# Kernel tuning notes

Hardware: AMD Instinct MI355X
Metric: run time of the kernel (lower is better)

The kernel has to match this reference:

```python
import jax, jax.numpy as jnp
import numpy as np

B, S, D, H = 4, 2048, 1024, 16
DH = D // H


def setup_inputs() -> dict:
    key = jax.random.key(0)
    ks = jax.random.split(key, 12)
    inv = 1.0 / np.sqrt(D)
    inp = {
        "queries": jax.random.normal(ks[0], (B, S, D), jnp.float32),
        "keys": jax.random.normal(ks[1], (B, S, D), jnp.float32),
        "values": jax.random.normal(ks[2], (B, S, D), jnp.float32),
        # causal mask: 1.0 where attention is disallowed (strictly upper triangle)
        "mask": jnp.triu(jnp.ones((S, S), jnp.float32), k=1)[None, None, :, :],
        "Wq": jax.random.normal(ks[3], (D, D), jnp.float32) * inv,
        "bq": jnp.zeros((D,), jnp.float32),
        "Wk": jax.random.normal(ks[4], (D, D), jnp.float32) * inv,
        "bk": jnp.zeros((D,), jnp.float32),
        "Wv": jax.random.normal(ks[5], (D, D), jnp.float32) * inv,
        "bv": jnp.zeros((D,), jnp.float32),
        "Wo": jax.random.normal(ks[6], (D, D), jnp.float32) * inv,
        "bo": jnp.zeros((D,), jnp.float32),
    }
    return inp


def _split_heads(x):
    # [B, S, D] -> [B, H, S, DH]
    b, s, _ = x.shape
    return x.reshape(b, s, H, DH).transpose(0, 2, 1, 3)


def reference(queries, keys, values, mask, Wq, bq, Wk, bk, Wv, bv, Wo, bo):
    q = _split_heads(queries @ Wq + bq)
    k = _split_heads(keys @ Wk + bk)
    v = _split_heads(values @ Wv + bv)
    scores = jnp.einsum("bhqd,bhkd->bhqk", q, k) / jnp.sqrt(jnp.float32(DH))
    scores = scores + mask * -1e9
    attn = jax.nn.softmax(scores, axis=-1)
    ctx = jnp.einsum("bhqk,bhkd->bhqd", attn, v)  # [B,H,S,DH]
    ctx = ctx.transpose(0, 2, 1, 3).reshape(queries.shape[0], -1, D)
    return ctx @ Wo + bo
```

## Files before the change

### kernel.cpp

```cpp
#include <hip/hip_runtime.h>
#include <hip/hip_bf16.h>

#define S_LEN 2048
#define DMODEL 1024
#define NHEAD 16
#define DHEAD 64
#define BATCH 4
#define MTOT (BATCH * S_LEN)

typedef __attribute__((ext_vector_type(8))) short short8;
typedef __attribute__((ext_vector_type(8))) unsigned short ushort8;
typedef __attribute__((ext_vector_type(4))) float f32x4;

__device__ __forceinline__ unsigned short f2bf(float x) {
    unsigned int u = __float_as_uint(x);
    u += 0x7FFFu + ((u >> 16) & 1u);
    return (unsigned short)(u >> 16);
}

__global__ __launch_bounds__(256) void k_conv_bf16(const float* __restrict__ src,
                                                   unsigned short* __restrict__ dst, int n8) {
    int i = blockIdx.x * 256 + threadIdx.x;
    if (i >= n8) return;
    const float4* s4 = (const float4*)src;
    float4 a = s4[(size_t)i * 2];
    float4 b = s4[(size_t)i * 2 + 1];
    ushort8 v;
    v[0] = f2bf(a.x); v[1] = f2bf(a.y); v[2] = f2bf(a.z); v[3] = f2bf(a.w);
    v[4] = f2bf(b.x); v[5] = f2bf(b.y); v[6] = f2bf(b.z); v[7] = f2bf(b.w);
    *(ushort8*)(dst + (size_t)i * 8) = v;
}

__global__ __launch_bounds__(256) void k_transpose_w(const float* __restrict__ W0, const float* __restrict__ W1,
                                                     const float* __restrict__ W2, const float* __restrict__ W3,
                                                     unsigned short* __restrict__ T0, unsigned short* __restrict__ T1,
                                                     unsigned short* __restrict__ T2, unsigned short* __restrict__ T3) {
    const float* src; unsigned short* dst;
    switch (blockIdx.z) {
        case 0: src = W0; dst = T0; break;
        case 1: src = W1; dst = T1; break;
        case 2: src = W2; dst = T2; break;
        default: src = W3; dst = T3; break;
    }
    __shared__ float t[32][33];
    int tx = threadIdx.x & 31, ty = threadIdx.x >> 5;
    int n0 = blockIdx.x * 32, k0 = blockIdx.y * 32;
#pragma unroll
    for (int i = 0; i < 32; i += 8)
        t[ty + i][tx] = src[(size_t)(k0 + ty + i) * DMODEL + n0 + tx];
    __syncthreads();
#pragma unroll
    for (int i = 0; i < 32; i += 8)
        dst[(size_t)(n0 + ty + i) * DMODEL + k0 + tx] = f2bf(t[tx][ty + i]);
}

template <int OUT_FP32>
__global__ __launch_bounds__(256) void k_gemm_nt(const unsigned short* __restrict__ A,
                                                 const unsigned short* __restrict__ Bt,
                                                 const float* __restrict__ bias,
                                                 void* __restrict__ Cout,
                                                 int M, int N, int K, float alpha) {
    __shared__ unsigned short Al[128 * 32];
    __shared__ unsigned short Bl[128 * 32];
    int tid = threadIdx.x;
    int wid = tid >> 6;
    int lane = tid & 63;
    int lr = lane & 15, lg = lane >> 4;
    int bm = blockIdx.y * 128, bn = blockIdx.x * 128;
    int wm = (wid >> 1) * 64, wn = (wid & 1) * 64;

    f32x4 acc[4][4];
#pragma unroll
    for (int mt = 0; mt < 4; ++mt)
#pragma unroll
        for (int nt = 0; nt < 4; ++nt) acc[mt][nt] = (f32x4)0.0f;

    for (int k0 = 0; k0 < K; k0 += 32) {
#pragma unroll
        for (int i = 0; i < 2; ++i) {
            int c = (wid * 2 + i) * 64 + lane;
            int row = c >> 2, cc = c & 3;
            const unsigned short* ga = A + (size_t)(bm + row) * K + k0 + cc * 8;
            const unsigned short* gb = Bt + (size_t)(bn + row) * K + k0 + cc * 8;
            __builtin_amdgcn_global_load_lds((const __attribute__((address_space(1))) unsigned int*)ga,
                                             (__attribute__((address_space(3))) unsigned int*)(Al + (wid * 2 + i) * 512),
                                             16, 0, 0);
            __builtin_amdgcn_global_load_lds((const __attribute__((address_space(1))) unsigned int*)gb,
                                             (__attribute__((address_space(3))) unsigned int*)(Bl + (wid * 2 + i) * 512),
                                             16, 0, 0);
        }
        __syncthreads();

        short8 af[4], bf[4];
#pragma unroll
        for (int mt = 0; mt < 4; ++mt)
            af[mt] = *(const short8*)(Al + (wm + mt * 16 + lr) * 32 + lg * 8);
#pragma unroll
        for (int nt = 0; nt < 4; ++nt)
            bf[nt] = *(const short8*)(Bl + (wn + nt * 16 + lr) * 32 + lg * 8);
#pragma unroll
        for (int mt = 0; mt < 4; ++mt)
#pragma unroll
            for (int nt = 0; nt < 4; ++nt)
                acc[mt][nt] = __builtin_amdgcn_mfma_f32_16x16x32_bf16(af[mt], bf[nt], acc[mt][nt], 0, 0, 0);
        __syncthreads();
    }

#pragma unroll
    for (int nt = 0; nt < 4; ++nt) {
        int col = bn + wn + nt * 16 + lr;
        float bv = bias[col];
#pragma unroll
        for (int mt = 0; mt < 4; ++mt) {
#pragma unroll
            for (int r = 0; r < 4; ++r) {
                int row = bm + wm + mt * 16 + lg * 4 + r;
                float v = (acc[mt][nt][r] + bv) * alpha;
                if (OUT_FP32)
                    ((float*)Cout)[(size_t)row * N + col] = v;
                else
                    ((unsigned short*)Cout)[(size_t)row * N + col] = f2bf(v);
            }
        }
    }
}

__global__ __launch_bounds__(64, 2) void k_attn(const unsigned short* __restrict__ Qp,
                                                const unsigned short* __restrict__ Kp,
                                                const unsigned short* __restrict__ Vp,
                                                unsigned short* __restrict__ Ctx) {
    int lane = threadIdx.x & 63;
    int lr = lane & 15, lg = lane >> 4;
    int qb = blockIdx.x;
    int bh = blockIdx.y;
    int b = bh >> 4, h = bh & 15;
    size_t baserow = (size_t)b * S_LEN;
    int hcol = h * DHEAD;

    short8 qf[4][2];
#pragma unroll
    for (int qt = 0; qt < 4; ++qt)
#pragma unroll
        for (int ks = 0; ks < 2; ++ks)
            qf[qt][ks] = *(const short8*)(Qp + (baserow + qb * 64 + qt * 16 + lr) * DMODEL + hcol + ks * 32 + lg * 8);

    f32x4 ctx[4][4];
#pragma unroll
    for (int dt = 0; dt < 4; ++dt)
#pragma unroll
        for (int qt = 0; qt < 4; ++qt) ctx[dt][qt] = (f32x4)0.0f;

    float mrun[4], lrun[4];
#pragma unroll
    for (int qt = 0; qt < 4; ++qt) { mrun[qt] = -1e30f; lrun[qt] = 0.0f; }

    for (int kb = 0; kb <= qb; ++kb) {
        f32x4 s[4][4];
#pragma unroll
        for (int kt = 0; kt < 4; ++kt)
#pragma unroll
            for (int qt = 0; qt < 4; ++qt) s[kt][qt] = (f32x4)0.0f;

#pragma unroll
        for (int kt = 0; kt < 4; ++kt) {
            short8 kf[2];
#pragma unroll
            for (int ks = 0; ks < 2; ++ks)
                kf[ks] = *(const short8*)(Kp + (baserow + kb * 64 + kt * 16 + lr) * DMODEL + hcol + ks * 32 + lg * 8);
#pragma unroll
            for (int qt = 0; qt < 4; ++qt)
#pragma unroll
                for (int ks = 0; ks < 2; ++ks)
                    s[kt][qt] = __builtin_amdgcn_mfma_f32_16x16x32_bf16(kf[ks], qf[qt][ks], s[kt][qt], 0, 0, 0);
        }

        if (kb == qb) {
#pragma unroll
            for (int kt = 0; kt < 4; ++kt)
#pragma unroll
                for (int qt = 0; qt < 4; ++qt)
#pragma unroll
                    for (int r = 0; r < 4; ++r)
                        if (kt * 16 + lg * 4 + r > qt * 16 + lr) s[kt][qt][r] = -1e30f;
        }

        short8 pf[4][2];
#pragma unroll
        for (int qt = 0; qt < 4; ++qt) {
            float mx = -1e30f;
#pragma unroll
            for (int kt = 0; kt < 4; ++kt)
#pragma unroll
                for (int r = 0; r < 4; ++r) mx = fmaxf(mx, s[kt][qt][r]);
            mx = fmaxf(mx, __shfl_xor(mx, 16));
            mx = fmaxf(mx, __shfl_xor(mx, 32));
            float mnew = fmaxf(mrun[qt], mx);
            float scale = __expf(mrun[qt] - mnew);
            mrun[qt] = mnew;
            float rs = 0.0f;
#pragma unroll
            for (int kt = 0; kt < 4; ++kt)
#pragma unroll
                for (int r = 0; r < 4; ++r) {
                    float p = __expf(s[kt][qt][r] - mnew);
                    s[kt][qt][r] = p;
                    rs += p;
                }
            rs += __shfl_xor(rs, 16);
            rs += __shfl_xor(rs, 32);
            lrun[qt] = lrun[qt] * scale + rs;
#pragma unroll
            for (int dt = 0; dt < 4; ++dt)
#pragma unroll
                for (int r = 0; r < 4; ++r) ctx[dt][qt][r] *= scale;
#pragma unroll
            for (int ks = 0; ks < 2; ++ks)
#pragma unroll
                for (int j = 0; j < 8; ++j)
                    pf[qt][ks][j] = (short)f2bf(s[2 * ks + (j >> 2)][qt][j & 3]);
        }

        const unsigned short* vbase = Vp + (baserow + kb * 64) * DMODEL + hcol + lr;
#pragma unroll
        for (int dt = 0; dt < 4; ++dt) {
#pragma unroll
            for (int ks = 0; ks < 2; ++ks) {
                short8 vf;
#pragma unroll
                for (int j = 0; j < 8; ++j) {
                    int kk = 32 * ks + 16 * (j >> 2) + 4 * lg + (j & 3);
                    vf[j] = (short)vbase[(size_t)kk * DMODEL + dt * 16];
                }
#pragma unroll
                for (int qt = 0; qt < 4; ++qt)
                    ctx[dt][qt] = __builtin_amdgcn_mfma_f32_16x16x32_bf16(vf, pf[qt][ks], ctx[dt][qt], 0, 0, 0);
            }
        }
    }

#pragma unroll
    for (int qt = 0; qt < 4; ++qt) {
        float inv = 1.0f / lrun[qt];
#pragma unroll
        for (int dt = 0; dt < 4; ++dt) {
            unsigned int lo = (unsigned int)f2bf(ctx[dt][qt][0] * inv) | ((unsigned int)f2bf(ctx[dt][qt][1] * inv) << 16);
            unsigned int hi = (unsigned int)f2bf(ctx[dt][qt][2] * inv) | ((unsigned int)f2bf(ctx[dt][qt][3] * inv) << 16);
            uint2 vv; vv.x = lo; vv.y = hi;
            *(uint2*)(Ctx + (baserow + qb * 64 + qt * 16 + lr) * DMODEL + hcol + dt * 16 + lg * 4) = vv;
        }
    }
}

extern "C" void kernel_launch(void* const* d_in, const int* in_sizes, int n_in,
                              void* d_out, int out_size, void* d_ws, size_t ws_size,
                              hipStream_t stream) {
    const float* q_in = (const float*)d_in[0];
    const float* k_in = (const float*)d_in[1];
    const float* v_in = (const float*)d_in[2];
    const float* Wq = (const float*)d_in[4];
    const float* bq = (const float*)d_in[5];
    const float* Wk = (const float*)d_in[6];
    const float* bk = (const float*)d_in[7];
    const float* Wv = (const float*)d_in[8];
    const float* bv = (const float*)d_in[9];
    const float* Wo = (const float*)d_in[10];
    const float* bo = (const float*)d_in[11];

    char* ws = (char*)d_ws;
    const size_t SZ_ACT = (size_t)MTOT * DMODEL * 2;
    const size_t SZ_W = (size_t)DMODEL * DMODEL * 2;
    unsigned short* Xq = (unsigned short*)(ws);
    unsigned short* Xk = (unsigned short*)(ws + SZ_ACT);
    unsigned short* Xv = (unsigned short*)(ws + 2 * SZ_ACT);
    unsigned short* Tq = (unsigned short*)(ws + 3 * SZ_ACT);
    unsigned short* Tk = (unsigned short*)(ws + 3 * SZ_ACT + SZ_W);
    unsigned short* Tv = (unsigned short*)(ws + 3 * SZ_ACT + 2 * SZ_W);
    unsigned short* To = (unsigned short*)(ws + 3 * SZ_ACT + 3 * SZ_W);
    unsigned short* Qp = (unsigned short*)(ws + 3 * SZ_ACT + 4 * SZ_W);
    unsigned short* Kp = (unsigned short*)(ws + 4 * SZ_ACT + 4 * SZ_W);
    unsigned short* Vp = (unsigned short*)(ws + 5 * SZ_ACT + 4 * SZ_W);
    unsigned short* Cx = (unsigned short*)(ws + 6 * SZ_ACT + 4 * SZ_W);

    int n8 = MTOT * DMODEL / 8;
    k_conv_bf16<<<(n8 + 255) / 256, 256, 0, stream>>>(q_in, Xq, n8);
    k_conv_bf16<<<(n8 + 255) / 256, 256, 0, stream>>>(k_in, Xk, n8);
    k_conv_bf16<<<(n8 + 255) / 256, 256, 0, stream>>>(v_in, Xv, n8);
    k_transpose_w<<<dim3(32, 32, 4), 256, 0, stream>>>(Wq, Wk, Wv, Wo, Tq, Tk, Tv, To);

    dim3 gg(DMODEL / 128, MTOT / 128);
    k_gemm_nt<0><<<gg, 256, 0, stream>>>(Xq, Tq, bq, Qp, MTOT, DMODEL, DMODEL, 0.125f);
    k_gemm_nt<0><<<gg, 256, 0, stream>>>(Xk, Tk, bk, Kp, MTOT, DMODEL, DMODEL, 1.0f);
    k_gemm_nt<0><<<gg, 256, 0, stream>>>(Xv, Tv, bv, Vp, MTOT, DMODEL, DMODEL, 1.0f);

    k_attn<<<dim3(S_LEN / 64, BATCH * NHEAD), 64, 0, stream>>>(Qp, Kp, Vp, Cx);

    k_gemm_nt<1><<<gg, 256, 0, stream>>>(Cx, To, bo, d_out, MTOT, DMODEL, DMODEL, 1.0f);
}
```

Measured before the change: 465.2 us.

## Batch QKV GEMMs, store V transposed, reorder attention blocks, add setprio

Merges the three conversion kernels into one launch and the three projection GEMMs into a single grid-z launch with a swizzled tile order. The V projection is written transposed per head, so the attention kernel loads V fragments with vector loads instead of strided scalar gathers, and those loads are hoisted before the softmax. Attention blocks are remapped so the longest causal query blocks start first and heads are spread across XCDs, occupancy is raised to 3, and s_setprio wraps the MFMA bursts. The V epilogue now does scattered 2-byte stores along the sequence stride, which may slow that GEMM's output writes.

```diff
diff --git a/kernel.cpp b/kernel.cpp
--- a/kernel.cpp
+++ b/kernel.cpp
@@ -10,6 +10,7 @@
 
 typedef __attribute__((ext_vector_type(8))) short short8;
 typedef __attribute__((ext_vector_type(8))) unsigned short ushort8;
+typedef __attribute__((ext_vector_type(4))) unsigned short ushort4v;
 typedef __attribute__((ext_vector_type(4))) float f32x4;
 
 __device__ __forceinline__ unsigned short f2bf(float x) {
@@ -18,10 +19,14 @@
     return (unsigned short)(u >> 16);
 }
 
-__global__ __launch_bounds__(256) void k_conv_bf16(const float* __restrict__ src,
-                                                   unsigned short* __restrict__ dst, int n8) {
+__global__ __launch_bounds__(256) void k_conv3(const float* __restrict__ s0, const float* __restrict__ s1,
+                                               const float* __restrict__ s2,
+                                               unsigned short* __restrict__ d0, unsigned short* __restrict__ d1,
+                                               unsigned short* __restrict__ d2, int n8) {
     int i = blockIdx.x * 256 + threadIdx.x;
     if (i >= n8) return;
+    const float* src = blockIdx.y == 0 ? s0 : (blockIdx.y == 1 ? s1 : s2);
+    unsigned short* dst = blockIdx.y == 0 ? d0 : (blockIdx.y == 1 ? d1 : d2);
     const float4* s4 = (const float4*)src;
     float4 a = s4[(size_t)i * 2];
     float4 b = s4[(size_t)i * 2 + 1];
@@ -54,19 +59,30 @@
         dst[(size_t)(n0 + ty + i) * DMODEL + k0 + tx] = f2bf(t[tx][ty + i]);
 }
 
-template <int OUT_FP32>
-__global__ __launch_bounds__(256) void k_gemm_nt(const unsigned short* __restrict__ A,
-                                                 const unsigned short* __restrict__ Bt,
-                                                 const float* __restrict__ bias,
-                                                 void* __restrict__ Cout,
-                                                 int M, int N, int K, float alpha) {
+__global__ __launch_bounds__(256) void k_gemm_qkv(const unsigned short* __restrict__ Xq,
+                                                  const unsigned short* __restrict__ Xk,
+                                                  const unsigned short* __restrict__ Xv,
+                                                  const unsigned short* __restrict__ Tq,
+                                                  const unsigned short* __restrict__ Tk,
+                                                  const unsigned short* __restrict__ Tv,
+                                                  const float* __restrict__ bqp, const float* __restrict__ bkp,
+                                                  const float* __restrict__ bvp,
+                                                  unsigned short* __restrict__ Qp, unsigned short* __restrict__ Kp,
+                                                  unsigned short* __restrict__ Vt) {
+    int z = blockIdx.z;
+    const unsigned short* A = z == 0 ? Xq : (z == 1 ? Xk : Xv);
+    const unsigned short* Bt = z == 0 ? Tq : (z == 1 ? Tk : Tv);
+    const float* bias = z == 0 ? bqp : (z == 1 ? bkp : bvp);
+    float alpha = z == 0 ? 0.125f : 1.0f;
+
     __shared__ unsigned short Al[128 * 32];
     __shared__ unsigned short Bl[128 * 32];
     int tid = threadIdx.x;
-    int wid = tid >> 6;
-    int lane = tid & 63;
+    int wid = tid >> 6, lane = tid & 63;
     int lr = lane & 15, lg = lane >> 4;
-    int bm = blockIdx.y * 128, bn = blockIdx.x * 128;
+    int lin = blockIdx.y * 8 + blockIdx.x;
+    int tile = (lin & 7) * 64 + (lin >> 3);
+    int bm = (tile >> 3) * 128, bn = (tile & 7) * 128;
     int wm = (wid >> 1) * 64, wn = (wid & 1) * 64;
 
     f32x4 acc[4][4];
@@ -75,13 +91,13 @@
 #pragma unroll
         for (int nt = 0; nt < 4; ++nt) acc[mt][nt] = (f32x4)0.0f;
 
-    for (int k0 = 0; k0 < K; k0 += 32) {
+    for (int k0 = 0; k0 < DMODEL; k0 += 32) {
 #pragma unroll
         for (int i = 0; i < 2; ++i) {
             int c = (wid * 2 + i) * 64 + lane;
             int row = c >> 2, cc = c & 3;
-            const unsigned short* ga = A + (size_t)(bm + row) * K + k0 + cc * 8;
-            const unsigned short* gb = Bt + (size_t)(bn + row) * K + k0 + cc * 8;
+            const unsigned short* ga = A + (size_t)(bm + row) * DMODEL + k0 + cc * 8;
+            const unsigned short* gb = Bt + (size_t)(bn + row) * DMODEL + k0 + cc * 8;
             __builtin_amdgcn_global_load_lds((const __attribute__((address_space(1))) unsigned int*)ga,
                                              (__attribute__((address_space(3))) unsigned int*)(Al + (wid * 2 + i) * 512),
                                              16, 0, 0);
@@ -90,7 +106,6 @@
                                              16, 0, 0);
         }
         __syncthreads();
-
         short8 af[4], bf[4];
 #pragma unroll
         for (int mt = 0; mt < 4; ++mt)
@@ -98,11 +113,13 @@
 #pragma unroll
         for (int nt = 0; nt < 4; ++nt)
             bf[nt] = *(const short8*)(Bl + (wn + nt * 16 + lr) * 32 + lg * 8);
+        __builtin_amdgcn_s_setprio(1);
 #pragma unroll
         for (int mt = 0; mt < 4; ++mt)
 #pragma unroll
             for (int nt = 0; nt < 4; ++nt)
                 acc[mt][nt] = __builtin_amdgcn_mfma_f32_16x16x32_bf16(af[mt], bf[nt], acc[mt][nt], 0, 0, 0);
+        __builtin_amdgcn_s_setprio(0);
         __syncthreads();
     }
 
@@ -116,23 +133,96 @@
             for (int r = 0; r < 4; ++r) {
                 int row = bm + wm + mt * 16 + lg * 4 + r;
                 float v = (acc[mt][nt][r] + bv) * alpha;
-                if (OUT_FP32)
-                    ((float*)Cout)[(size_t)row * N + col] = v;
-                else
-                    ((unsigned short*)Cout)[(size_t)row * N + col] = f2bf(v);
+                if (z < 2) {
+                    unsigned short* dst = z == 0 ? Qp : Kp;
+                    dst[(size_t)row * DMODEL + col] = f2bf(v);
+                } else {
+                    int h = col >> 6, d = col & 63;
+                    int b = row >> 11, s = row & 2047;
+                    Vt[((size_t)(b * NHEAD + h) * DHEAD + d) * S_LEN + s] = f2bf(v);
+                }
             }
         }
     }
 }
 
-__global__ __launch_bounds__(64, 2) void k_attn(const unsigned short* __restrict__ Qp,
+__global__ __launch_bounds__(256) void k_gemm_out(const unsigned short* __restrict__ A,
+                                                  const unsigned short* __restrict__ Bt,
+                                                  const float* __restrict__ bias,
+                                                  float* __restrict__ Cout) {
+    __shared__ unsigned short Al[128 * 32];
+    __shared__ unsigned short Bl[128 * 32];
+    int tid = threadIdx.x;
+    int wid = tid >> 6, lane = tid & 63;
+    int lr = lane & 15, lg = lane >> 4;
+    int lin = blockIdx.y * 8 + blockIdx.x;
+    int tile = (lin & 7) * 64 + (lin >> 3);
+    int bm = (tile >> 3) * 128, bn = (tile & 7) * 128;
+    int wm = (wid >> 1) * 64, wn = (wid & 1) * 64;
+
+    f32x4 acc[4][4];
+#pragma unroll
+    for (int mt = 0; mt < 4; ++mt)
+#pragma unroll
+        for (int nt = 0; nt < 4; ++nt) acc[mt][nt] = (f32x4)0.0f;
+
+    for (int k0 = 0; k0 < DMODEL; k0 += 32) {
+#pragma unroll
+        for (int i = 0; i < 2; ++i) {
+            int c = (wid * 2 + i) * 64 + lane;
+            int row = c >> 2, cc = c & 3;
+            const unsigned short* ga = A + (size_t)(bm + row) * DMODEL + k0 + cc * 8;
+            const unsigned short* gb = Bt + (size_t)(bn + row) * DMODEL + k0 + cc * 8;
+            __builtin_amdgcn_global_load_lds((const __attribute__((address_space(1))) unsigned int*)ga,
+                                             (__attribute__((address_space(3))) unsigned int*)(Al + (wid * 2 + i) * 512),
+                                             16, 0, 0);
+            __builtin_amdgcn_global_load_lds((const __attribute__((address_space(1))) unsigned int*)gb,
+                                             (__attribute__((address_space(3))) unsigned int*)(Bl + (wid * 2 + i) * 512),
+                                             16, 0, 0);
+        }
+        __syncthreads();
+        short8 af[4], bf[4];
+#pragma unroll
+        for (int mt = 0; mt < 4; ++mt)
+            af[mt] = *(const short8*)(Al + (wm + mt * 16 + lr) * 32 + lg * 8);
+#pragma unroll
+        for (int nt = 0; nt < 4; ++nt)
+            bf[nt] = *(const short8*)(Bl + (wn + nt * 16 + lr) * 32 + lg * 8);
+        __builtin_amdgcn_s_setprio(1);
+#pragma unroll
+        for (int mt = 0; mt < 4; ++mt)
+#pragma unroll
+            for (int nt = 0; nt < 4; ++nt)
+                acc[mt][nt] = __builtin_amdgcn_mfma_f32_16x16x32_bf16(af[mt], bf[nt], acc[mt][nt], 0, 0, 0);
+        __builtin_amdgcn_s_setprio(0);
+        __syncthreads();
+    }
+
+#pragma unroll
+    for (int nt = 0; nt < 4; ++nt) {
+        int col = bn + wn + nt * 16 + lr;
+        float bv = bias[col];
+#pragma unroll
+        for (int mt = 0; mt < 4; ++mt)
+#pragma unroll
+            for (int r = 0; r < 4; ++r) {
+                int row = bm + wm + mt * 16 + lg * 4 + r;
+                Cout[(size_t)row * DMODEL + col] = acc[mt][nt][r] + bv;
+            }
+    }
+}
+
+__global__ __launch_bounds__(64, 3) void k_attn(const unsigned short* __restrict__ Qp,
                                                 const unsigned short* __restrict__ Kp,
-                                                const unsigned short* __restrict__ Vp,
+                                                const unsigned short* __restrict__ Vt,
                                                 unsigned short* __restrict__ Ctx) {
     int lane = threadIdx.x & 63;
     int lr = lane & 15, lg = lane >> 4;
-    int qb = blockIdx.x;
-    int bh = blockIdx.y;
+    int bid = blockIdx.x;
+    int xcd = bid & 7;
+    int j = bid >> 3;
+    int bh = xcd + 8 * (j & 7);
+    int qb = (S_LEN / 64 - 1) - (j >> 3);
     int b = bh >> 4, h = bh & 15;
     size_t baserow = (size_t)b * S_LEN;
     int hcol = h * DHEAD;
@@ -154,24 +244,43 @@
 #pragma unroll
     for (int qt = 0; qt < 4; ++qt) { mrun[qt] = -1e30f; lrun[qt] = 0.0f; }
 
+    const unsigned short* vth = Vt + (size_t)bh * DHEAD * S_LEN;
+
     for (int kb = 0; kb <= qb; ++kb) {
         f32x4 s[4][4];
 #pragma unroll
         for (int kt = 0; kt < 4; ++kt)
 #pragma unroll
             for (int qt = 0; qt < 4; ++qt) s[kt][qt] = (f32x4)0.0f;
-
 #pragma unroll
         for (int kt = 0; kt < 4; ++kt) {
             short8 kf[2];
 #pragma unroll
             for (int ks = 0; ks < 2; ++ks)
                 kf[ks] = *(const short8*)(Kp + (baserow + kb * 64 + kt * 16 + lr) * DMODEL + hcol + ks * 32 + lg * 8);
+            __builtin_amdgcn_s_setprio(1);
 #pragma unroll
             for (int qt = 0; qt < 4; ++qt)
 #pragma unroll
                 for (int ks = 0; ks < 2; ++ks)
                     s[kt][qt] = __builtin_amdgcn_mfma_f32_16x16x32_bf16(kf[ks], qf[qt][ks], s[kt][qt], 0, 0, 0);
+            __builtin_amdgcn_s_setprio(0);
+        }
+
+        short8 vf[4][2];
+        {
+            const unsigned short* vb = vth + (size_t)kb * 64 + 4 * lg;
+#pragma unroll
+            for (int dt = 0; dt < 4; ++dt)
+#pragma unroll
+                for (int ks = 0; ks < 2; ++ks) {
+                    ushort4v lo = *(const ushort4v*)(vb + (size_t)(dt * 16 + lr) * S_LEN + 32 * ks);
+                    ushort4v hi = *(const ushort4v*)(vb + (size_t)(dt * 16 + lr) * S_LEN + 32 * ks + 16);
+                    short8 t;
+                    t[0] = (short)lo[0]; t[1] = (short)lo[1]; t[2] = (short)lo[2]; t[3] = (short)lo[3];
+                    t[4] = (short)hi[0]; t[5] = (short)hi[1]; t[6] = (short)hi[2]; t[7] = (short)hi[3];
+                    vf[dt][ks] = t;
+                }
         }
 
         if (kb == qb) {
@@ -216,26 +325,19 @@
 #pragma unroll
             for (int ks = 0; ks < 2; ++ks)
 #pragma unroll
-                for (int j = 0; j < 8; ++j)
-                    pf[qt][ks][j] = (short)f2bf(s[2 * ks + (j >> 2)][qt][j & 3]);
-        }
-
-        const unsigned short* vbase = Vp + (baserow + kb * 64) * DMODEL + hcol + lr;
-#pragma unroll
-        for (int dt = 0; dt < 4; ++dt) {
-#pragma unroll
-            for (int ks = 0; ks < 2; ++ks) {
-                short8 vf;
-#pragma unroll
-                for (int j = 0; j < 8; ++j) {
-                    int kk = 32 * ks + 16 * (j >> 2) + 4 * lg + (j & 3);
-                    vf[j] = (short)vbase[(size_t)kk * DMODEL + dt * 16];
-                }
+                for (int jj = 0; jj < 8; ++jj)
+                    pf[qt][ks][jj] = (short)f2bf(s[2 * ks + (jj >> 2)][qt][jj & 3]);
+        }
+
+        __builtin_amdgcn_s_setprio(1);
+#pragma unroll
+        for (int dt = 0; dt < 4; ++dt)
+#pragma unroll
+            for (int ks = 0; ks < 2; ++ks)
 #pragma unroll
                 for (int qt = 0; qt < 4; ++qt)
-                    ctx[dt][qt] = __builtin_amdgcn_mfma_f32_16x16x32_bf16(vf, pf[qt][ks], ctx[dt][qt], 0, 0, 0);
-            }
-        }
+                    ctx[dt][qt] = __builtin_amdgcn_mfma_f32_16x16x32_bf16(vf[dt][ks], pf[qt][ks], ctx[dt][qt], 0, 0, 0);
+        __builtin_amdgcn_s_setprio(0);
     }
 
 #pragma unroll
@@ -278,21 +380,16 @@
     unsigned short* To = (unsigned short*)(ws + 3 * SZ_ACT + 3 * SZ_W);
     unsigned short* Qp = (unsigned short*)(ws + 3 * SZ_ACT + 4 * SZ_W);
     unsigned short* Kp = (unsigned short*)(ws + 4 * SZ_ACT + 4 * SZ_W);
-    unsigned short* Vp = (unsigned short*)(ws + 5 * SZ_ACT + 4 * SZ_W);
+    unsigned short* Vt = (unsigned short*)(ws + 5 * SZ_ACT + 4 * SZ_W);
     unsigned short* Cx = (unsigned short*)(ws + 6 * SZ_ACT + 4 * SZ_W);
 
     int n8 = MTOT * DMODEL / 8;
-    k_conv_bf16<<<(n8 + 255) / 256, 256, 0, stream>>>(q_in, Xq, n8);
-    k_conv_bf16<<<(n8 + 255) / 256, 256, 0, stream>>>(k_in, Xk, n8);
-    k_conv_bf16<<<(n8 + 255) / 256, 256, 0, stream>>>(v_in, Xv, n8);
+    k_conv3<<<dim3((n8 + 255) / 256, 3), 256, 0, stream>>>(q_in, k_in, v_in, Xq, Xk, Xv, n8);
     k_transpose_w<<<dim3(32, 32, 4), 256, 0, stream>>>(Wq, Wk, Wv, Wo, Tq, Tk, Tv, To);
 
-    dim3 gg(DMODEL / 128, MTOT / 128);
-    k_gemm_nt<0><<<gg, 256, 0, stream>>>(Xq, Tq, bq, Qp, MTOT, DMODEL, DMODEL, 0.125f);
-    k_gemm_nt<0><<<gg, 256, 0, stream>>>(Xk, Tk, bk, Kp, MTOT, DMODEL, DMODEL, 1.0f);
-    k_gemm_nt<0><<<gg, 256, 0, stream>>>(Xv, Tv, bv, Vp, MTOT, DMODEL, DMODEL, 1.0f);
-
-    k_attn<<<dim3(S_LEN / 64, BATCH * NHEAD), 64, 0, stream>>>(Qp, Kp, Vp, Cx);
-
-    k_gemm_nt<1><<<gg, 256, 0, stream>>>(Cx, To, bo, d_out, MTOT, DMODEL, DMODEL, 1.0f);
-}
+    k_gemm_qkv<<<dim3(8, 64, 3), 256, 0, stream>>>(Xq, Xk, Xv, Tq, Tk, Tv, bq, bk, bv, Qp, Kp, Vt);
+
+    k_attn<<<dim3((S_LEN / 64) * BATCH * NHEAD), 64, 0, stream>>>(Qp, Kp, Vt, Cx);
+
+    k_gemm_out<<<dim3(8, 64), 256, 0, stream>>>(Cx, To, bo, (float*)d_out);
+}
```

Result: slower. 520.1 us (+11.8%).
